# Kernel optimization log

Measured on AMD Instinct MI355X. Metric: run time of the kernel, lower is better.

The kernel has to match this reference:

```python
import jax, jax.numpy as jnp
import numpy as np

NEG_SLOPE = 0.2
EPS = 1e-16


def _add_self_loops(edge_index, edge_weight, N):
    # PyG add_self_loops with fill_value='mean': self-loop attr = mean of
    # incoming edge attrs per node (0 if node has no incoming edges).
    src, dst = edge_index[0], edge_index[1]
    ones = jnp.ones_like(edge_weight)
    cnt = jax.ops.segment_sum(ones, dst, num_segments=N)
    wsum = jax.ops.segment_sum(edge_weight, dst, num_segments=N)
    self_w = jnp.where(cnt > 0, wsum / jnp.maximum(cnt, 1.0), 0.0)
    loop = jnp.arange(N, dtype=src.dtype)
    return (jnp.concatenate([src, loop]), jnp.concatenate([dst, loop]),
            jnp.concatenate([edge_weight, self_w]))


def _gatv2_layer(x, src, dst, ew, Wl, Wr, att, We, bias, N):
    # x: [M, N, Din]; src/dst: [E']; ew: [E']; att: [H, C]
    M = x.shape[0]
    H, C = att.shape
    xl = (x @ Wl).reshape(M, N, H, C)   # source transform (lin_l)
    xr = (x @ Wr).reshape(M, N, H, C)   # target transform (lin_r)
    xj = xl[:, src]                      # [M, E', H, C] gather source feats
    xi = xr[:, dst]                      # [M, E', H, C] gather target feats
    ee = (ew[:, None] @ We).reshape(-1, H, C)  # [E', H, C] edge embedding
    s = jax.nn.leaky_relu(xi + xj + ee[None], NEG_SLOPE)
    logits = jnp.einsum('mehc,hc->meh', s, att)  # [M, E', H]
    # segment softmax over edges grouped by destination node
    smax = jax.vmap(lambda u: jax.ops.segment_max(u, dst, num_segments=N))(logits)
    a = jnp.exp(logits - smax[:, dst])
    denom = jax.vmap(lambda u: jax.ops.segment_sum(u, dst, num_segments=N))(a)
    alpha = a / (denom[:, dst] + EPS)
    msg = alpha[..., None] * xj          # [M, E', H, C]
    out = jax.vmap(lambda u: jax.ops.segment_sum(u, dst, num_segments=N))(msg)
    return out.reshape(M, N, H * C) + bias


def setup_inputs() -> dict:
    key = jax.random.key(0)
    ks = jax.random.split(key, 14)
    B, T, N, Din = 2, 8, 5000, 64
    E, H, OUT = 80000, 2, 128
    C = OUT // H  # 64
    g = jax.nn.initializers.glorot_uniform()
    inp = {
        'x': jax.random.normal(ks[0], (B, T, N, Din), jnp.float32),
        'edge_index': jax.random.randint(ks[1], (2, E), 0, N, jnp.int32),
        'edge_weight': jax.random.uniform(ks[2], (E,), jnp.float32),
        # conv1 params
        'Wl1': g(ks[3], (Din, H * C), jnp.float32),
        'Wr1': g(ks[4], (Din, H * C), jnp.float32),
        'att1': g(ks[5], (H, C), jnp.float32),
        'We1': g(ks[6], (1, H * C), jnp.float32),
        'b1': jnp.zeros((H * C,), jnp.float32),
        # conv2 params
        'Wl2': g(ks[7], (OUT, H * C), jnp.float32),
        'Wr2': g(ks[8], (OUT, H * C), jnp.float32),
        'att2': g(ks[9], (H, C), jnp.float32),
        'We2': g(ks[10], (1, H * C), jnp.float32),
        'b2': jnp.zeros((H * C,), jnp.float32),
    }
    return inp


def reference(x, edge_index, edge_weight, Wl1, Wr1, att1, We1, b1,
              Wl2, Wr2, att2, We2, b2):
    B, T, N, Din = x.shape
    M = B * T
    # Tiling edges by B*T with node offsets is equivalent to sharing the same
    # edge list across M independent graph copies -> vectorize over M.
    src, dst, ew = _add_self_loops(edge_index, edge_weight, N)
    h = x.reshape(M, N, Din)
    h = _gatv2_layer(h, src, dst, ew, Wl1, Wr1, att1, We1, b1, N)
    h = jax.nn.elu(h)
    h = _gatv2_layer(h, src, dst, ew, Wl2, Wr2, att2, We2, b2, N)
    h = jax.nn.elu(h)
    return h.reshape(B, T, N, -1)
```

## Files before the change

### kernel.cpp

```cpp
#include <hip/hip_runtime.h>
#include <cstdint>
#include <cstddef>

static constexpr float NEG_SLOPE_C = 0.2f;
static constexpr float EPS_C = 1e-16f;
static constexpr float LOG2E_C = 1.4426950408889634f;

#if defined(__has_builtin)
#if __has_builtin(__builtin_amdgcn_exp2f)
#define EXP2F(x) __builtin_amdgcn_exp2f(x)
#else
#define EXP2F(x) exp2f(x)
#endif
#else
#define EXP2F(x) exp2f(x)
#endif

typedef __attribute__((ext_vector_type(8))) short bf16x8;
typedef __attribute__((ext_vector_type(4))) float f32x4;
typedef __attribute__((ext_vector_type(2))) float f32x2;

__device__ __forceinline__ f32x2 pk_add(f32x2 a, f32x2 b) {
    f32x2 d;
    asm("v_pk_add_f32 %0, %1, %2" : "=v"(d) : "v"(a), "v"(b));
    return d;
}
__device__ __forceinline__ f32x2 pk_mul(f32x2 a, f32x2 b) {
    f32x2 d;
    asm("v_pk_mul_f32 %0, %1, %2" : "=v"(d) : "v"(a), "v"(b));
    return d;
}
__device__ __forceinline__ f32x2 pk_fma(f32x2 a, f32x2 b, f32x2 c) {
    f32x2 d;
    asm("v_pk_fma_f32 %0, %1, %2, %3" : "=v"(d) : "v"(a), "v"(b), "v"(c));
    return d;
}
__device__ __forceinline__ f32x2 pk_abs(f32x2 a) {
    f32x2 d;
    d.x = __builtin_fabsf(a.x);
    d.y = __builtin_fabsf(a.y);
    return d;
}

__device__ __forceinline__ short bf16_rne(float x) {
    unsigned u = __float_as_uint(x);
    u = (u + 0x7FFF + ((u >> 16) & 1)) >> 16;
    return (short)u;
}
__device__ __forceinline__ float bf16f(short s) {
    return __uint_as_float(((unsigned)(unsigned short)s) << 16);
}

template<int CTRL>
__device__ __forceinline__ float dpp_add_f(float v) {
    int x = __builtin_amdgcn_update_dpp(0, __float_as_int(v), CTRL, 0xf, 0xf, true);
    return v + __int_as_float(x);
}

__device__ __forceinline__ float reduce16(float q) {
    q = dpp_add_f<0xB1>(q);
    q = dpp_add_f<0x4E>(q);
    q = dpp_add_f<0x141>(q);
    q = dpp_add_f<0x140>(q);
    return q;
}


__global__ void degree_kernel(const int* __restrict__ ei, const float* __restrict__ ew,
                              int E, int* __restrict__ cnt, float* __restrict__ wsum) {
    int e = blockIdx.x * blockDim.x + threadIdx.x;
    if (e >= E) return;
    int dst = ei[E + e];
    atomicAdd(&cnt[dst], 1);
    atomicAdd(&wsum[dst], ew[e]);
}

__global__ void scan_kernel(const int* __restrict__ cnt, const float* __restrict__ wsum,
                            int N, int E, int* __restrict__ offs, float* __restrict__ self_w) {
    __shared__ int bufA[1024];
    __shared__ int bufB[1024];
    int t = threadIdx.x;
    int chunk = (N + 1023) / 1024;
    int lo = t * chunk;
    int hi = lo + chunk; if (hi > N) hi = N; if (lo > N) lo = N;
    int s = 0;
    for (int n = lo; n < hi; ++n) s += cnt[n];
    bufA[t] = s;
    __syncthreads();
    int* srcb = bufA; int* dstb = bufB;
    for (int d = 1; d < 1024; d <<= 1) {
        int v = srcb[t];
        if (t >= d) v += srcb[t - d];
        dstb[t] = v;
        __syncthreads();
        int* tmp = srcb; srcb = dstb; dstb = tmp;
    }
    int run = (t == 0) ? 0 : srcb[t - 1];
    for (int n = lo; n < hi; ++n) { offs[n] = run; run += cnt[n]; }
    if (t == 0) offs[N] = E;
    for (int n = t; n < N; n += 1024) {
        int c = cnt[n];
        self_w[n] = (c > 0) ? (wsum[n] / (float)c) : 0.0f;
    }
}

__global__ void scatter_kernel(const int* __restrict__ ei, const float* __restrict__ ew, int E,
                               const int* __restrict__ offs, int* __restrict__ cursor,
                               int2* __restrict__ pairs) {
    int e = blockIdx.x * blockDim.x + threadIdx.x;
    if (e >= E) return;
    int dst = ei[E + e];
    int pos = offs[dst] + atomicAdd(&cursor[dst], 1);
    pairs[pos] = make_int2(ei[e] * 512, __float_as_int(ew[e]));
}


template<int K>
__global__ void wprep_kernel(const float* __restrict__ Wl, const float* __restrict__ Wr,
                             uint4* __restrict__ Wf) {
    const int gid = blockIdx.x * 256 + threadIdx.x;
    const int lane = gid & 63;
    const int t = (gid >> 6) & 15;
    const int s = gid >> 10;
    const int mr = lane & 15, q = lane >> 4;
    const int col = t * 16 + mr;
    const float* src = (col < 128) ? (Wl + col) : (Wr + col - 128);
    union { short sh[8]; uint4 u; } hv, lv;
    #pragma unroll
    for (int j = 0; j < 8; ++j) {
        const float v = src[(size_t)(s * 32 + q * 8 + j) * 128];
        const short h = bf16_rne(v);
        hv.sh[j] = h;
        lv.sh[j] = bf16_rne(v - bf16f(h));
    }
    const size_t base = (size_t)s * 2048 + (size_t)(t * 2) * 64 + lane;
    Wf[base] = hv.u;
    Wf[base + 64] = lv.u;
}


template<int K>
__global__ __launch_bounds__(256) void gemm_mfma_kernel(
    const float* __restrict__ X, const uint4* __restrict__ Wf,
    float* __restrict__ outL, float* __restrict__ outR) {
    __shared__ uint4 wbuf[2048];
    const int tid = threadIdx.x;
    const int wv = tid >> 6;
    const int lane = tid & 63;
    const int q = lane >> 4;
    const int mr = lane & 15;
    const int xrow = blockIdx.x * 64 + wv * 16 + mr;

    f32x4 acc[16];
    #pragma unroll
    for (int t = 0; t < 16; ++t) acc[t] = (f32x4){0.f, 0.f, 0.f, 0.f};

    const float* xp = X + (size_t)xrow * K + q * 8;

    for (int s = 0; s < K / 32; ++s) {
        const float4 a0 = *(const float4*)(xp + s * 32);
        const float4 a1 = *(const float4*)(xp + s * 32 + 4);

        __syncthreads();
        const uint4* gsrc = Wf + (size_t)s * 2048 + wv * 512 + lane;
        #pragma unroll
        for (int i = 0; i < 8; ++i)
            wbuf[wv * 512 + i * 64 + lane] = gsrc[i * 64];
        __syncthreads();

        const float av[8] = {a0.x, a0.y, a0.z, a0.w, a1.x, a1.y, a1.z, a1.w};
        bf16x8 xh, xl;
        #pragma unroll
        for (int j = 0; j < 8; ++j) {
            const short h = bf16_rne(av[j]);
            xh[j] = h;
            xl[j] = bf16_rne(av[j] - bf16f(h));
        }
        #pragma unroll
        for (int t = 0; t < 16; ++t) {
            const bf16x8 wh = *(const bf16x8*)&wbuf[(t * 2) * 64 + lane];
            const bf16x8 wl = *(const bf16x8*)&wbuf[(t * 2 + 1) * 64 + lane];
            acc[t] = __builtin_amdgcn_mfma_f32_16x16x32_bf16(wh, xh, acc[t], 0, 0, 0);
            acc[t] = __builtin_amdgcn_mfma_f32_16x16x32_bf16(wl, xh, acc[t], 0, 0, 0);
            acc[t] = __builtin_amdgcn_mfma_f32_16x16x32_bf16(wh, xl, acc[t], 0, 0, 0);
        }
    }

    const size_t ob = (size_t)xrow * 128 + q * 4;
    #pragma unroll
    for (int t = 0; t < 8; ++t) {
        *(float4*)(outL + ob + t * 16) =
            make_float4(acc[t][0], acc[t][1], acc[t][2], acc[t][3]);
        *(float4*)(outR + ob + t * 16) =
            make_float4(acc[t + 8][0], acc[t + 8][1], acc[t + 8][2], acc[t + 8][3]);
    }
}


__global__ __launch_bounds__(256) void edge_kernel(
    const float* __restrict__ xl, const float* __restrict__ xr,
    const int* __restrict__ offs, const int2* __restrict__ pairs,
    const float* __restrict__ self_w,
    const float* __restrict__ att, const float* __restrict__ We,
    const float* __restrict__ bias, float* __restrict__ out,
    int N, int M) {
    const int wave = __builtin_amdgcn_readfirstlane(threadIdx.x >> 6);
    const int b = blockIdx.x;
    const int hb = (b >= 10000) ? (b - 10000) : b;
    const int m = ((b >= 10000) ? 8 : 0) + (hb & 7);
    const int n = (hb >> 3) * 4 + wave;
    if (n >= N) return;
    const int lane = threadIdx.x & 63;
    const int j = lane & 31;
    const bool hi = lane >= 32;
    const int h4 = (lane >> 5) << 2;
    const int j16 = j << 4;

    const char* xlp = (const char*)(xl + (size_t)m * N * 128);
    const char* xrp = (const char*)(xr + (size_t)m * N * 128);

    const int beg = offs[n], end = offs[n + 1];
    const int last = end - 1;
    const bool any = end > beg;

    int2 myp;
    if (any) myp = pairs[min(beg + lane, last)];

    f32x2 a06_01, a06_23, a04_01, a04_23, we01, we23, xi01, xi23;
    {
        const float4 at4 = ((const float4*)att)[j];
        const float4 we4 = ((const float4*)We)[j];
        const float4 xi4 = *(const float4*)(xrp + (size_t)n * 512 + j16);
        const float c06 = 0.6f * LOG2E_C, c04 = 0.4f * LOG2E_C;
        a06_01 = (f32x2){at4.x * c06, at4.y * c06};
        a06_23 = (f32x2){at4.z * c06, at4.w * c06};
        a04_01 = (f32x2){at4.x * c04, at4.y * c04};
        a04_23 = (f32x2){at4.z * c04, at4.w * c04};
        we01 = (f32x2){we4.x, we4.y};
        we23 = (f32x2){we4.z, we4.w};
        xi01 = (f32x2){xi4.x, xi4.y};
        xi23 = (f32x2){xi4.z, xi4.w};
    }

    float base, lsum;
    f32x2 acc01, acc23;
    {
        const float sw = self_w[n];
        const f32x2 sw2 = (f32x2){sw, sw};
        const float4 xj4 = *(const float4*)(xlp + (size_t)n * 512 + j16);
        const f32x2 s01 = pk_fma(sw2, we01, pk_add(xi01, (f32x2){xj4.x, xj4.y}));
        const f32x2 s23 = pk_fma(sw2, we23, pk_add(xi23, (f32x2){xj4.z, xj4.w}));
        f32x2 q01 = pk_mul(a06_01, s01);
        q01 = pk_fma(a04_01, pk_abs(s01), q01);
        f32x2 q23 = pk_mul(a06_23, s23);
        q23 = pk_fma(a04_23, pk_abs(s23), q23);
        const f32x2 qp = pk_add(q01, q23);
        base = reduce16(qp.x + qp.y);
        lsum = 0.5f;
        acc01 = (f32x2){xj4.x * 0.5f, xj4.y * 0.5f};
        acc23 = (f32x2){xj4.z * 0.5f, xj4.w * 0.5f};
    }

    auto BODY = [&](f32x2 w2, float4 xj4, bool mask) {
        const f32x2 xj01 = (f32x2){xj4.x, xj4.y};
        const f32x2 xj23 = (f32x2){xj4.z, xj4.w};
        const f32x2 s01 = pk_fma(w2, we01, pk_add(xi01, xj01));
        const f32x2 s23 = pk_fma(w2, we23, pk_add(xi23, xj23));
        f32x2 q01 = pk_mul(a06_01, s01);
        q01 = pk_fma(a04_01, pk_abs(s01), q01);
        f32x2 q23 = pk_mul(a06_23, s23);
        q23 = pk_fma(a04_23, pk_abs(s23), q23);
        const f32x2 qp = pk_add(q01, q23);
        const float q = reduce16(qp.x + qp.y);
        float t = EXP2F(q - base);
        if (mask) t = hi ? 0.f : t;
        lsum += t;
        const f32x2 t2 = (f32x2){t, t};
        acc01 = pk_fma(t2, xj01, acc01);
        acc23 = pk_fma(t2, xj23, acc23);
    };

    if (any) {
        for (int cbeg = beg; cbeg < end; cbeg += 64) {
            const int cdeg = min(end - cbeg, 64);
            const int niter = (cdeg + 1) >> 1;
            const bool odd = (cdeg & 1) != 0;

            auto PULL = [&](int s, int& ro, f32x2& w2) {
                const int idx = (s << 3) + h4;
                ro = __builtin_amdgcn_ds_bpermute(idx, myp.x);
                const int wb = __builtin_amdgcn_ds_bpermute(idx, myp.y);
                w2.x = __int_as_float(wb);
                w2.y = w2.x;
            };
            auto GATH = [&](int ro) -> float4 {
                return *(const float4*)(xlp + (unsigned)(ro + j16));
            };

            int roA, roB, roC, roD;
            f32x2 wA, wB, wC, wD;
            PULL(0, roA, wA);
            PULL(1, roB, wB);
            PULL(2, roC, wC);
            PULL(3, roD, wD);
            float4 xA = GATH(roA);
            float4 xB = GATH(roB);
            float4 xC, xD;

            int k = 0;
            while (k + 4 < niter) {
                xC = GATH(roC);
                xD = GATH(roD);
                __builtin_amdgcn_sched_barrier(0);
                BODY(wA, xA, false);
                PULL(k + 4, roA, wA);
                BODY(wB, xB, false);
                PULL(k + 5, roB, wB);
                xA = GATH(roA);
                xB = GATH(roB);
                __builtin_amdgcn_sched_barrier(0);
                BODY(wC, xC, false);
                PULL(k + 6, roC, wC);
                BODY(wD, xD, false);
                PULL(k + 7, roD, wD);
                k += 4;
            }
            const int rem = niter - k;
            if (rem >= 3) xC = GATH(roC);
            if (rem == 4) xD = GATH(roD);
            BODY(wA, xA, odd && (rem == 1));
            if (rem >= 2) BODY(wB, xB, odd && (rem == 2));
            if (rem >= 3) BODY(wC, xC, odd && (rem == 3));
            if (rem == 4) BODY(wD, xD, odd);

            if (cbeg + 64 < end)
                myp = pairs[min(cbeg + 64 + lane, last)];
        }
    }

    lsum += __shfl_xor(lsum, 32, 64);
    acc01.x += __shfl_xor(acc01.x, 32, 64);
    acc01.y += __shfl_xor(acc01.y, 32, 64);
    acc23.x += __shfl_xor(acc23.x, 32, 64);
    acc23.y += __shfl_xor(acc23.y, 32, 64);

    const float inv = 1.f / (lsum + EPS_C);
    const float4 b4 = ((const float4*)bias)[j];
    float o0 = fmaf(acc01.x, inv, b4.x);
    float o1 = fmaf(acc01.y, inv, b4.y);
    float o2 = fmaf(acc23.x, inv, b4.z);
    float o3 = fmaf(acc23.y, inv, b4.w);
    o0 = o0 > 0.f ? o0 : (__expf(o0) - 1.f);
    o1 = o1 > 0.f ? o1 : (__expf(o1) - 1.f);
    o2 = o2 > 0.f ? o2 : (__expf(o2) - 1.f);
    o3 = o3 > 0.f ? o3 : (__expf(o3) - 1.f);
    if (!hi) {
        ((float4*)(out + (size_t)m * N * 128))[n * 32 + j] =
            make_float4(o0, o1, o2, o3);
    }
}


extern "C" void kernel_launch(void* const* d_in, const int* in_sizes, int n_in,
                              void* d_out, int out_size, void* d_ws, size_t ws_size,
                              hipStream_t stream) {
    const float* x    = (const float*)d_in[0];
    const int*   ei   = (const int*)d_in[1];
    const float* ew   = (const float*)d_in[2];
    const float* Wl1  = (const float*)d_in[3];
    const float* Wr1  = (const float*)d_in[4];
    const float* att1 = (const float*)d_in[5];
    const float* We1  = (const float*)d_in[6];
    const float* b1   = (const float*)d_in[7];
    const float* Wl2  = (const float*)d_in[8];
    const float* Wr2  = (const float*)d_in[9];
    const float* att2 = (const float*)d_in[10];
    const float* We2  = (const float*)d_in[11];
    const float* b2   = (const float*)d_in[12];

    const int E = in_sizes[1] / 2;
    const int N = 5000;
    const int R = out_size / 128;
    const int M = R / N;

    char* ws = (char*)d_ws;
    size_t off = 0;
    auto alloc = [&](size_t bytes) {
        char* p = ws + off;
        off = (off + bytes + 255) & ~(size_t)255;
        return p;
    };
    int*   cnt    = (int*)  alloc((size_t)N * 4);
    float* wsum   = (float*)alloc((size_t)N * 4);
    int*   cursor = (int*)  alloc((size_t)N * 4);
    float* selfw  = (float*)alloc((size_t)N * 4);
    int*   offs   = (int*)  alloc((size_t)(N + 1) * 4);
    int2*  pairs  = (int2*) alloc((size_t)(E + 1) * 8);
    uint4* wf1    = (uint4*)alloc((size_t)2 * 2048 * 16);
    uint4* wf2    = (uint4*)alloc((size_t)4 * 2048 * 16);
    float* bufA   = (float*)alloc((size_t)R * 128 * 4);
    float* bufB   = (float*)alloc((size_t)R * 128 * 4);
    float* bufC   = (float*)alloc((size_t)R * 128 * 4);

    const size_t zspan = (size_t)((char*)cursor - (char*)cnt) + (size_t)N * 4;
    hipMemsetAsync(cnt, 0, zspan, stream);

    int eb = (E + 255) / 256;
    degree_kernel<<<eb, 256, 0, stream>>>(ei, ew, E, cnt, wsum);
    scan_kernel<<<1, 1024, 0, stream>>>(cnt, wsum, N, E, offs, selfw);
    scatter_kernel<<<eb, 256, 0, stream>>>(ei, ew, E, offs, cursor, pairs);
    wprep_kernel<64><<<8, 256, 0, stream>>>(Wl1, Wr1, wf1);
    wprep_kernel<128><<<16, 256, 0, stream>>>(Wl2, Wr2, wf2);

    const int gb = R / 64;
    const int tb = 2 * ((N + 3) / 4) * 8;

    gemm_mfma_kernel<64><<<gb, 256, 0, stream>>>(x, wf1, bufA, bufB);
    edge_kernel<<<tb, 256, 0, stream>>>(bufA, bufB, offs, pairs, selfw,
                                        att1, We1, b1, bufC, N, M);
    gemm_mfma_kernel<128><<<gb, 256, 0, stream>>>(bufC, wf2, bufA, bufB);
    edge_kernel<<<tb, 256, 0, stream>>>(bufA, bufB, offs, pairs, selfw,
                                        att2, We2, b2, (float*)d_out, N, M);
}
```

Measured before the change: 291.9 us.

## Restructure MFMA GEMM to share X tiles in LDS and split weight columns across waves

The GEMM kernel no longer stages the full weight slice in shared memory for all waves. Instead, each wave converts a slice of the X tile to hi/lo bf16 and stores it in LDS, then computes a 4x4 output tile covering all 64 rows of the block and a quarter of the 256 output columns. Weights are read directly from global memory per wave. This cuts LDS traffic and bf16 conversion per block and gives more MFMA reuse per loaded operand. In exchange it relies on L1/L2 caching for the direct global weight loads, and each wave's stores cover a different output layout.

```diff
diff --git a/kernel.cpp b/kernel.cpp
--- a/kernel.cpp
+++ b/kernel.cpp
@@ -143,56 +143,73 @@
 __global__ __launch_bounds__(256) void gemm_mfma_kernel(
     const float* __restrict__ X, const uint4* __restrict__ Wf,
     float* __restrict__ outL, float* __restrict__ outR) {
-    __shared__ uint4 wbuf[2048];
+    __shared__ uint4 xbuf[8 * 64];
     const int tid = threadIdx.x;
-    const int wv = tid >> 6;
+    const int w = tid >> 6;
     const int lane = tid & 63;
     const int q = lane >> 4;
     const int mr = lane & 15;
-    const int xrow = blockIdx.x * 64 + wv * 16 + mr;
-
-    f32x4 acc[16];
+    const int blockRow = blockIdx.x * 64;
+
+    const int srow = lane;
+    const float* sxp = X + (size_t)(blockRow + srow) * K + w * 8;
+    const int sdst = ((srow >> 4) * 2) * 64 + w * 16 + (srow & 15);
+
+    f32x4 acc[4][4];
     #pragma unroll
-    for (int t = 0; t < 16; ++t) acc[t] = (f32x4){0.f, 0.f, 0.f, 0.f};
-
-    const float* xp = X + (size_t)xrow * K + q * 8;
+    for (int tt = 0; tt < 4; ++tt)
+        #pragma unroll
+        for (int r = 0; r < 4; ++r)
+            acc[tt][r] = (f32x4){0.f, 0.f, 0.f, 0.f};
 
     for (int s = 0; s < K / 32; ++s) {
-        const float4 a0 = *(const float4*)(xp + s * 32);
-        const float4 a1 = *(const float4*)(xp + s * 32 + 4);
-
+        const float4 a0 = *(const float4*)(sxp + s * 32);
+        const float4 a1 = *(const float4*)(sxp + s * 32 + 4);
+        union { short sh[8]; uint4 u; } hv, lv;
+        {
+            const float av[8] = {a0.x, a0.y, a0.z, a0.w, a1.x, a1.y, a1.z, a1.w};
+            #pragma unroll
+            for (int jj = 0; jj < 8; ++jj) {
+                const short h = bf16_rne(av[jj]);
+                hv.sh[jj] = h;
+                lv.sh[jj] = bf16_rne(av[jj] - bf16f(h));
+            }
+        }
         __syncthreads();
-        const uint4* gsrc = Wf + (size_t)s * 2048 + wv * 512 + lane;
+        xbuf[sdst] = hv.u;
+        xbuf[sdst + 64] = lv.u;
+        __syncthreads();
+
+        bf16x8 xh[4], xl[4];
         #pragma unroll
-        for (int i = 0; i < 8; ++i)
-            wbuf[wv * 512 + i * 64 + lane] = gsrc[i * 64];
-        __syncthreads();
-
-        const float av[8] = {a0.x, a0.y, a0.z, a0.w, a1.x, a1.y, a1.z, a1.w};
-        bf16x8 xh, xl;
+        for (int r = 0; r < 4; ++r) {
+            xh[r] = *(const bf16x8*)&xbuf[(r * 2) * 64 + lane];
+            xl[r] = *(const bf16x8*)&xbuf[(r * 2 + 1) * 64 + lane];
+        }
+        const uint4* wp = Wf + (size_t)s * 2048 + (size_t)(4 * w) * 128 + lane;
         #pragma unroll
-        for (int j = 0; j < 8; ++j) {
-            const short h = bf16_rne(av[j]);
-            xh[j] = h;
-            xl[j] = bf16_rne(av[j] - bf16f(h));
+        for (int tt = 0; tt < 4; ++tt) {
+            const bf16x8 wh = *(const bf16x8*)&wp[tt * 128];
+            const bf16x8 wl = *(const bf16x8*)&wp[tt * 128 + 64];
+            #pragma unroll
+            for (int r = 0; r < 4; ++r) {
+                acc[tt][r] = __builtin_amdgcn_mfma_f32_16x16x32_bf16(wh, xh[r], acc[tt][r], 0, 0, 0);
+                acc[tt][r] = __builtin_amdgcn_mfma_f32_16x16x32_bf16(wl, xh[r], acc[tt][r], 0, 0, 0);
+                acc[tt][r] = __builtin_amdgcn_mfma_f32_16x16x32_bf16(wh, xl[r], acc[tt][r], 0, 0, 0);
+            }
         }
+    }
+
+    float* const obase = (w < 2) ? outL : outR;
+    const int cbase = (w & 1) * 64 + q * 4;
+    #pragma unroll
+    for (int tt = 0; tt < 4; ++tt) {
         #pragma unroll
-        for (int t = 0; t < 16; ++t) {
-            const bf16x8 wh = *(const bf16x8*)&wbuf[(t * 2) * 64 + lane];
-            const bf16x8 wl = *(const bf16x8*)&wbuf[(t * 2 + 1) * 64 + lane];
-            acc[t] = __builtin_amdgcn_mfma_f32_16x16x32_bf16(wh, xh, acc[t], 0, 0, 0);
-            acc[t] = __builtin_amdgcn_mfma_f32_16x16x32_bf16(wl, xh, acc[t], 0, 0, 0);
-            acc[t] = __builtin_amdgcn_mfma_f32_16x16x32_bf16(wh, xl, acc[t], 0, 0, 0);
+        for (int r = 0; r < 4; ++r) {
+            const size_t o = (size_t)(blockRow + r * 16 + mr) * 128 + cbase + tt * 16;
+            *(float4*)(obase + o) =
+                make_float4(acc[tt][r][0], acc[tt][r][1], acc[tt][r][2], acc[tt][r][3]);
         }
-    }
-
-    const size_t ob = (size_t)xrow * 128 + q * 4;
-    #pragma unroll
-    for (int t = 0; t < 8; ++t) {
-        *(float4*)(outL + ob + t * 16) =
-            make_float4(acc[t][0], acc[t][1], acc[t][2], acc[t][3]);
-        *(float4*)(outR + ob + t * 16) =
-            make_float4(acc[t + 8][0], acc[t + 8][1], acc[t + 8][2], acc[t + 8][3]);
     }
 }
 
```

Measured after the change: 283.7 us. 2.8% less time.
